# Kernel tuning notes

Measured on AMD Instinct MI355X. Metric: run time of the kernel, lower is better.

Reference implementation:

```python
import jax, jax.numpy as jnp
import numpy as np


def setup_inputs() -> dict:
    key = jax.random.key(0)
    k1, k2 = jax.random.split(key)
    x = jax.random.normal(k1, (16, 512, 64, 64), dtype=jnp.float32)
    gamma = jax.random.normal(k2, (1,), dtype=jnp.float32) * 0.05  # 'random_normal' init
    return {"x": x, "gamma": gamma}


def reference(x, gamma):
    # x: (B, C, H, W); code path is channels_last, C taken from x.shape[1]
    B, C, H, W = x.shape
    N = H * W
    # Reshape((-1, C)) is a flat row-major reshape -> (B, N, C)
    q = x.reshape(B, N, C)  # query == key == value (same tensor)
    # energy = matmul(query, key, transpose_a=True) -> (B, C, C)
    energy = jnp.einsum('bnc,bnd->bcd', q, q)
    # reduce_max(energy, axis=1, keepdims=True)[0]: max over axis 1 then take
    # FIRST BATCH element -> shape (1, C), broadcast against (B, C, C)
    mx = jnp.max(energy, axis=1, keepdims=True)[0]  # (1, C)
    energy_2 = mx - energy  # (B, C, C)
    # Keras Activation('softmax') -> softmax over last axis
    attention = jax.nn.softmax(energy_2, axis=-1)  # (B, C, C)
    # matmul(attention, value, transpose_b=True): (B,C,C) @ (B,C,N) -> (B,C,N)
    out = jnp.einsum('bcd,bnd->bcn', attention, q)
    # Reshape back to x.shape[1:] = (C, H, W) (flat reshape, N = H*W)
    out = out.reshape(B, C, H, W)
    return gamma * out + x
```

## Files before the change

kernel.cpp:

```cpp
#include <hip/hip_runtime.h>
#include <cstdint>

#define B_DIM 16
#define C_DIM 512
#define N_DIM 4096

typedef __bf16 bf16x8 __attribute__((ext_vector_type(8)));
typedef unsigned short u16x8 __attribute__((ext_vector_type(8)));
typedef unsigned short u16x4 __attribute__((ext_vector_type(4)));
typedef unsigned int u32x4 __attribute__((ext_vector_type(4)));
typedef unsigned int u32x2 __attribute__((ext_vector_type(2)));
typedef float f32x4 __attribute__((ext_vector_type(4)));

__device__ __forceinline__ bf16x8 as_bf(u16x8 v) { return __builtin_bit_cast(bf16x8, v); }

__device__ __forceinline__ unsigned pack_hi(unsigned ua, unsigned ub) {
    return __builtin_amdgcn_perm(ub, ua, 0x07060302u);
}
__device__ __forceinline__ unsigned rne_pack(float a, float b) {
    unsigned ua = __float_as_uint(a);
    ua += 0x7fffu + ((ua >> 16) & 1u);
    unsigned ub = __float_as_uint(b);
    ub += 0x7fffu + ((ub >> 16) & 1u);
    return pack_hi(ua, ub);
}

#define BT 128
#define BK 32
#define BKP 40

__global__ __launch_bounds__(256) void gram_kernel(const float* __restrict__ x,
                                                   float* __restrict__ part, int kshift) {
    const int nwg = 10 * gridDim.z;
    const int chunk = nwg >> 3;
    const int flat = blockIdx.x + 10 * blockIdx.z;
    const int swz = (flat & 7) * chunk + (flat >> 3);
    const int tile = swz % 10;
    const int z = swz / 10;
    const int s = z & ((1 << kshift) - 1);
    const int b = z >> kshift;
    static const int TI[10] = {0, 0, 0, 0, 1, 1, 1, 2, 2, 3};
    static const int TJ[10] = {0, 1, 2, 3, 1, 2, 3, 2, 3, 3};
    const int c0 = TI[tile] * BT;
    const int d0 = TJ[tile] * BT;
    const bool diag = (c0 == d0);

    const float* __restrict__ Q = x + (size_t)b * (N_DIM * C_DIM);
    float* __restrict__ E = part + ((size_t)s * B_DIM + b) * (C_DIM * C_DIM);

    __shared__ unsigned short lAh[BT][BKP];
    __shared__ unsigned short lAl[BT][BKP];
    __shared__ unsigned short lBh[BT][BKP];
    __shared__ unsigned short lBl[BT][BKP];

    const int tid = threadIdx.x;
    const int lane = tid & 63;
    const int w = tid >> 6;
    const int moff = (w & 1) * 64;
    const int noff = (w >> 1) * 64;
    const int frow = lane & 15;
    const int fk = (lane >> 4) * 8;

    f32x4 acc[4][4];
#pragma unroll
    for (int m = 0; m < 4; ++m)
#pragma unroll
        for (int n = 0; n < 4; ++n) acc[m][n] = (f32x4){0.f, 0.f, 0.f, 0.f};

    const int cc = tid & 127;
    const int kh = tid >> 7;

    const int klen = N_DIM >> kshift;
    const float* gA = Q + (size_t)(s * klen + kh * 16) * C_DIM + (c0 + cc);
    const float* gB = Q + (size_t)(s * klen + kh * 16) * C_DIM + (d0 + cc);

    const unsigned short(*pBh)[BKP] = diag ? lAh : lBh;
    const unsigned short(*pBl)[BKP] = diag ? lAl : lBl;

    float av[16], bv[16];
#pragma unroll
    for (int i = 0; i < 16; ++i) av[i] = gA[(size_t)i * C_DIM];
    if (!diag) {
#pragma unroll
        for (int i = 0; i < 16; ++i) bv[i] = gB[(size_t)i * C_DIM];
    }
    gA += (size_t)BK * C_DIM;
    gB += (size_t)BK * C_DIM;

    const int T = klen / BK;
    for (int t = 0; t < T; ++t) {
        u32x4 ah[2], al[2], bh[2], bl[2];
#pragma unroll
        for (int g = 0; g < 2; ++g)
#pragma unroll
            for (int p = 0; p < 4; ++p) {
                const int j = g * 8 + p * 2;
                unsigned u0 = __float_as_uint(av[j]), u1 = __float_as_uint(av[j + 1]);
                ah[g][p] = pack_hi(u0, u1);
                float r0 = av[j] - __uint_as_float(u0 & 0xffff0000u);
                float r1 = av[j + 1] - __uint_as_float(u1 & 0xffff0000u);
                al[g][p] = pack_hi(__float_as_uint(r0), __float_as_uint(r1));
            }
        if (!diag) {
#pragma unroll
            for (int g = 0; g < 2; ++g)
#pragma unroll
                for (int p = 0; p < 4; ++p) {
                    const int j = g * 8 + p * 2;
                    unsigned u0 = __float_as_uint(bv[j]), u1 = __float_as_uint(bv[j + 1]);
                    bh[g][p] = pack_hi(u0, u1);
                    float r0 = bv[j] - __uint_as_float(u0 & 0xffff0000u);
                    float r1 = bv[j + 1] - __uint_as_float(u1 & 0xffff0000u);
                    bl[g][p] = pack_hi(__float_as_uint(r0), __float_as_uint(r1));
                }
        }

        __syncthreads();
        *(u16x8*)&lAh[cc][kh * 16]     = __builtin_bit_cast(u16x8, ah[0]);
        *(u16x8*)&lAh[cc][kh * 16 + 8] = __builtin_bit_cast(u16x8, ah[1]);
        *(u16x8*)&lAl[cc][kh * 16]     = __builtin_bit_cast(u16x8, al[0]);
        *(u16x8*)&lAl[cc][kh * 16 + 8] = __builtin_bit_cast(u16x8, al[1]);
        if (!diag) {
            *(u16x8*)&lBh[cc][kh * 16]     = __builtin_bit_cast(u16x8, bh[0]);
            *(u16x8*)&lBh[cc][kh * 16 + 8] = __builtin_bit_cast(u16x8, bh[1]);
            *(u16x8*)&lBl[cc][kh * 16]     = __builtin_bit_cast(u16x8, bl[0]);
            *(u16x8*)&lBl[cc][kh * 16 + 8] = __builtin_bit_cast(u16x8, bl[1]);
        }
        __syncthreads();

        if (t + 1 < T) {
#pragma unroll
            for (int i = 0; i < 16; ++i) av[i] = gA[(size_t)i * C_DIM];
            if (!diag) {
#pragma unroll
                for (int i = 0; i < 16; ++i) bv[i] = gB[(size_t)i * C_DIM];
            }
            gA += (size_t)BK * C_DIM;
            gB += (size_t)BK * C_DIM;
        }

        bf16x8 fbh[4], fbl[4];
#pragma unroll
        for (int n = 0; n < 4; ++n) {
            fbh[n] = as_bf(*(const u16x8*)&pBh[noff + n * 16 + frow][fk]);
            fbl[n] = as_bf(*(const u16x8*)&pBl[noff + n * 16 + frow][fk]);
        }
#pragma unroll
        for (int m = 0; m < 4; ++m) {
            bf16x8 fah = as_bf(*(const u16x8*)&lAh[moff + m * 16 + frow][fk]);
            bf16x8 fal = as_bf(*(const u16x8*)&lAl[moff + m * 16 + frow][fk]);
#pragma unroll
            for (int n = 0; n < 4; ++n) {
                acc[m][n] = __builtin_amdgcn_mfma_f32_16x16x32_bf16(fah, fbh[n], acc[m][n], 0, 0, 0);
                acc[m][n] = __builtin_amdgcn_mfma_f32_16x16x32_bf16(fah, fbl[n], acc[m][n], 0, 0, 0);
                acc[m][n] = __builtin_amdgcn_mfma_f32_16x16x32_bf16(fal, fbh[n], acc[m][n], 0, 0, 0);
            }
        }
    }

#pragma unroll
    for (int m = 0; m < 4; ++m)
#pragma unroll
        for (int n = 0; n < 4; ++n) {
            const int r = c0 + moff + m * 16 + (lane >> 4) * 4;
            const int col = d0 + noff + n * 16 + frow;
#pragma unroll
            for (int i = 0; i < 4; ++i)
                E[(size_t)(r + i) * C_DIM + col] = acc[m][n][i];
        }
    if (!diag) {
#pragma unroll
        for (int m = 0; m < 4; ++m)
#pragma unroll
            for (int n = 0; n < 4; ++n) {
                const int r = c0 + moff + m * 16 + (lane >> 4) * 4;
                const int col = d0 + noff + n * 16 + frow;
#pragma unroll
                for (int i = 0; i < 4; ++i)
                    E[(size_t)col * C_DIM + (r + i)] = acc[m][n][i];
            }
    }
}

__global__ __launch_bounds__(256) void colmax1(const float* __restrict__ part,
                                               float* __restrict__ pmax, int sk) {
    const int d = blockIdx.x * 256 + threadIdx.x;
    const int cg = blockIdx.y;
    const size_t PS = (size_t)B_DIM * C_DIM * C_DIM;
    float m = -3.4e38f;
    for (int c = cg * 16; c < cg * 16 + 16; ++c) {
        float e = 0.f;
        for (int s = 0; s < sk; ++s) e += part[(size_t)s * PS + (size_t)c * C_DIM + d];
        m = fmaxf(m, e);
    }
    pmax[cg * C_DIM + d] = m;
}

__global__ __launch_bounds__(256) void colmax2(const float* __restrict__ pmax,
                                               float* __restrict__ mx) {
    const int d = blockIdx.x * 256 + threadIdx.x;
    float m = pmax[d];
#pragma unroll
    for (int g = 1; g < 32; ++g) m = fmaxf(m, pmax[g * C_DIM + d]);
    mx[d] = m;
}

__global__ __launch_bounds__(256) void softmax_kernel(float* __restrict__ part,
                                                      const float* __restrict__ mx, int sk) {
    const int wid = blockIdx.x * 4 + (threadIdx.x >> 6);
    const int lane = threadIdx.x & 63;
    const size_t PS = (size_t)B_DIM * C_DIM * C_DIM;

    f32x4 ea = (f32x4){0.f, 0.f, 0.f, 0.f}, eb = ea;
    for (int s = 0; s < sk; ++s) {
        const f32x4* row = (const f32x4*)(part + (size_t)s * PS + (size_t)wid * C_DIM + lane * 8);
        ea += row[0];
        eb += row[1];
    }
    f32x4 ma = *(const f32x4*)&mx[lane * 8];
    f32x4 mb = *(const f32x4*)&mx[lane * 8 + 4];

    float v[8];
#pragma unroll
    for (int j = 0; j < 4; ++j) v[j] = ma[j] - ea[j];
#pragma unroll
    for (int j = 0; j < 4; ++j) v[4 + j] = mb[j] - eb[j];

    float rm = v[0];
#pragma unroll
    for (int j = 1; j < 8; ++j) rm = fmaxf(rm, v[j]);
#pragma unroll
    for (int st = 1; st < 64; st <<= 1) rm = fmaxf(rm, __shfl_xor(rm, st));

    float p[8];
    float sum = 0.f;
#pragma unroll
    for (int j = 0; j < 8; ++j) {
        p[j] = expf(v[j] - rm);
        sum += p[j];
    }
#pragma unroll
    for (int st = 1; st < 64; st <<= 1) sum += __shfl_xor(sum, st);

    const float inv = 1.f / sum;
    u32x4 o;
#pragma unroll
    for (int q = 0; q < 4; ++q) o[q] = rne_pack(p[2 * q] * inv, p[2 * q + 1] * inv);
    unsigned short* arow = (unsigned short*)part + (size_t)wid * 1024 + 512;
    *(u16x8*)&arow[lane * 8] = __builtin_bit_cast(u16x8, o);
}

__global__ __launch_bounds__(256) void gemm2_kernel(const unsigned short* __restrict__ att16,
                                                    const float* __restrict__ x,
                                                    const float* __restrict__ gamma,
                                                    float* __restrict__ out) {
    const int flat = blockIdx.x;
    const int swz = (flat & 7) * 256 + (flat >> 3);
    const int c0 = (swz & 3) * BT;
    const int n0 = ((swz >> 2) & 31) * BT;
    const int b = swz >> 7;

    const float* __restrict__ Q = x + (size_t)b * (N_DIM * C_DIM);
    float* __restrict__ Ob = out + (size_t)b * (C_DIM * N_DIM);
    const unsigned short* __restrict__ Ab = att16 + (size_t)(b * C_DIM + c0) * 1024 + 512;

    __shared__ unsigned short lA[2][BT][BKP];
    __shared__ unsigned short lB[2][BT][BKP];

    const int tid = threadIdx.x;
    const int lane = tid & 63;
    const int w = tid >> 6;
    const int moff = (w & 1) * 64;
    const int noff = (w >> 1) * 64;
    const int frow = lane & 15;
    const int fq = lane >> 4;
    const int fk = fq * 8;

    f32x4 acc[4][4];
#pragma unroll
    for (int m = 0; m < 4; ++m)
#pragma unroll
        for (int n = 0; n < 4; ++n) acc[m][n] = (f32x4){0.f, 0.f, 0.f, 0.f};

    const int ar = tid >> 2;
    const int ak = (tid & 3) * 8;
    const int br = tid >> 3;
    const int bk = (tid & 7) * 4;

    u16x8 pa[2];
    float4 rb[4];
#pragma unroll
    for (int i = 0; i < 2; ++i)
        pa[i] = *(const u16x8*)&Ab[(size_t)(ar + 64 * i) * 1024 + ak];
#pragma unroll
    for (int i = 0; i < 4; ++i)
        rb[i] = *(const float4*)&Q[(size_t)(n0 + br + 32 * i) * C_DIM + bk];
#pragma unroll
    for (int i = 0; i < 2; ++i)
        *(u16x8*)&lA[0][ar + 64 * i][ak] = pa[i];
#pragma unroll
    for (int i = 0; i < 4; ++i) {
        u32x2 pk = {pack_hi(__float_as_uint(rb[i].x), __float_as_uint(rb[i].y)),
                    pack_hi(__float_as_uint(rb[i].z), __float_as_uint(rb[i].w))};
        *(u16x4*)&lB[0][br + 32 * i][bk] = __builtin_bit_cast(u16x4, pk);
    }

    int cur = 0;
    for (int t = 0; t < 16; ++t) {
        __syncthreads();
        if (t < 15) {
            const int k1 = (t + 1) * BK;
#pragma unroll
            for (int i = 0; i < 2; ++i)
                pa[i] = *(const u16x8*)&Ab[(size_t)(ar + 64 * i) * 1024 + k1 + ak];
#pragma unroll
            for (int i = 0; i < 4; ++i)
                rb[i] = *(const float4*)&Q[(size_t)(n0 + br + 32 * i) * C_DIM + k1 + bk];
        }

        bf16x8 fb[4];
#pragma unroll
        for (int n = 0; n < 4; ++n)
            fb[n] = as_bf(*(const u16x8*)&lB[cur][noff + n * 16 + frow][fk]);
#pragma unroll
        for (int m = 0; m < 4; ++m) {
            const bf16x8 fa = as_bf(*(const u16x8*)&lA[cur][moff + m * 16 + frow][fk]);
#pragma unroll
            for (int n = 0; n < 4; ++n)
                acc[m][n] = __builtin_amdgcn_mfma_f32_16x16x32_bf16(fa, fb[n], acc[m][n], 0, 0, 0);
        }

        if (t < 15) {
            const int nb = cur ^ 1;
#pragma unroll
            for (int i = 0; i < 2; ++i)
                *(u16x8*)&lA[nb][ar + 64 * i][ak] = pa[i];
#pragma unroll
            for (int i = 0; i < 4; ++i) {
                u32x2 pk = {pack_hi(__float_as_uint(rb[i].x), __float_as_uint(rb[i].y)),
                            pack_hi(__float_as_uint(rb[i].z), __float_as_uint(rb[i].w))};
                *(u16x4*)&lB[nb][br + 32 * i][bk] = __builtin_bit_cast(u16x4, pk);
            }
        }
        cur ^= 1;
    }

    const float g = gamma[0];
#pragma unroll
    for (int m = 0; m < 4; ++m)
#pragma unroll
        for (int n = 0; n < 4; ++n) {
            const int r = c0 + moff + m * 16 + fq * 4;
            const int col = n0 + noff + n * 16 + frow;
#pragma unroll
            for (int i = 0; i < 4; ++i) {
                const size_t idx = (size_t)(r + i) * N_DIM + col;
                Ob[idx] = g * acc[m][n][i] + Q[idx];
            }
        }
}

extern "C" void kernel_launch(void* const* d_in, const int* in_sizes, int n_in,
                              void* d_out, int out_size, void* d_ws, size_t ws_size,
                              hipStream_t stream) {
    const float* x = (const float*)d_in[0];
    const float* gamma = (const float*)d_in[1];
    float* out = (float*)d_out;

    const size_t HDR = 128 * 1024;
    const size_t PSZ = (size_t)B_DIM * C_DIM * C_DIM * sizeof(float);
    int kshift = 0;
    if (ws_size >= HDR + 8 * PSZ) kshift = 3;
    else if (ws_size >= HDR + 4 * PSZ) kshift = 2;
    else if (ws_size >= HDR + 2 * PSZ) kshift = 1;
    const int SK = 1 << kshift;

    float* mx = (float*)d_ws;
    float* pmax = mx + C_DIM;
    float* part = (float*)((char*)d_ws + HDR);

    dim3 g1(10, 1, B_DIM * SK);
    gram_kernel<<<g1, 256, 0, stream>>>(x, part, kshift);

    colmax1<<<dim3(2, 32), 256, 0, stream>>>(part, pmax, SK);
    colmax2<<<2, 256, 0, stream>>>(pmax, mx);

    softmax_kernel<<<(B_DIM * C_DIM) / 4, 256, 0, stream>>>(part, mx, SK);

    gemm2_kernel<<<2048, 256, 0, stream>>>((const unsigned short*)part, x, gamma, out);
}
```

Before: 246.7 us.

## Emit bf16 copy of x in gram kernel; feed gemm2 via direct global-to-LDS loads

The diagonal gram tiles now write a truncated bf16 copy of x to workspace as a side effect. gemm2 reads that half-size copy instead of reading fp32 x and converting it, and it loads both operands with global_load_lds straight into an XOR-swizzled, unpadded shared buffer. This halves gemm2's B-operand traffic and removes register staging and conversion work. The cost is extra global writes in the gram kernel and a larger workspace, which may lower the split-K factor. The bf16 copy also uses truncation rather than round-to-nearest.

New measurement: 344.3 us. 39.5% more time.

```diff
diff --git a/kernel.cpp b/kernel.cpp
--- a/kernel.cpp
+++ b/kernel.cpp
@@ -25,12 +25,19 @@
     return pack_hi(ua, ub);
 }
 
+__device__ __forceinline__ void gload_lds16(const void* g, void* l) {
+    __builtin_amdgcn_global_load_lds((const __attribute__((address_space(1))) void*)g,
+                                     (__attribute__((address_space(3))) void*)l, 16, 0, 0);
+}
+
 #define BT 128
 #define BK 32
 #define BKP 40
 
 __global__ __launch_bounds__(256) void gram_kernel(const float* __restrict__ x,
-                                                   float* __restrict__ part, int kshift) {
+                                                   float* __restrict__ part,
+                                                   unsigned short* __restrict__ xbf,
+                                                   int kshift) {
     const int nwg = 10 * gridDim.z;
     const int chunk = nwg >> 3;
     const int flat = blockIdx.x + 10 * blockIdx.z;
@@ -73,6 +80,8 @@
     const int klen = N_DIM >> kshift;
     const float* gA = Q + (size_t)(s * klen + kh * 16) * C_DIM + (c0 + cc);
     const float* gB = Q + (size_t)(s * klen + kh * 16) * C_DIM + (d0 + cc);
+    unsigned short* gW = xbf + (size_t)b * (N_DIM * C_DIM) +
+                         (size_t)(s * klen + kh * 16) * C_DIM + (c0 + cc);
 
     const unsigned short(*pBh)[BKP] = diag ? lAh : lBh;
     const unsigned short(*pBl)[BKP] = diag ? lAl : lBl;
@@ -113,6 +122,12 @@
                     float r1 = bv[j + 1] - __uint_as_float(u1 & 0xffff0000u);
                     bl[g][p] = pack_hi(__float_as_uint(r0), __float_as_uint(r1));
                 }
+        } else {
+#pragma unroll
+            for (int i = 0; i < 16; ++i)
+                gW[(size_t)i * C_DIM] =
+                    (unsigned short)(__float_as_uint(av[i]) >> 16);
+            gW += (size_t)BK * C_DIM;
         }
 
         __syncthreads();
@@ -251,6 +266,7 @@
 }
 
 __global__ __launch_bounds__(256) void gemm2_kernel(const unsigned short* __restrict__ att16,
+                                                    const unsigned short* __restrict__ xbf,
                                                     const float* __restrict__ x,
                                                     const float* __restrict__ gamma,
                                                     float* __restrict__ out) {
@@ -260,12 +276,13 @@
     const int n0 = ((swz >> 2) & 31) * BT;
     const int b = swz >> 7;
 
-    const float* __restrict__ Q = x + (size_t)b * (N_DIM * C_DIM);
+    const float* __restrict__ Xf = x + (size_t)b * (N_DIM * C_DIM);
     float* __restrict__ Ob = out + (size_t)b * (C_DIM * N_DIM);
     const unsigned short* __restrict__ Ab = att16 + (size_t)(b * C_DIM + c0) * 1024 + 512;
-
-    __shared__ unsigned short lA[2][BT][BKP];
-    __shared__ unsigned short lB[2][BT][BKP];
+    const unsigned short* __restrict__ Bb = xbf + ((size_t)b * N_DIM + n0) * C_DIM;
+
+    __shared__ unsigned short lA[2][BT][BK];
+    __shared__ unsigned short lB[2][BT][BK];
 
     const int tid = threadIdx.x;
     const int lane = tid & 63;
@@ -274,7 +291,10 @@
     const int noff = (w >> 1) * 64;
     const int frow = lane & 15;
     const int fq = lane >> 4;
-    const int fk = fq * 8;
+    const int sfr = (fq ^ (frow & 3)) * 8;
+
+    const int sr = tid >> 2;
+    const int sc = (((tid & 3) ^ ((tid >> 2) & 3)) << 3);
 
     f32x4 acc[4][4];
 #pragma unroll
@@ -282,66 +302,42 @@
 #pragma unroll
         for (int n = 0; n < 4; ++n) acc[m][n] = (f32x4){0.f, 0.f, 0.f, 0.f};
 
-    const int ar = tid >> 2;
-    const int ak = (tid & 3) * 8;
-    const int br = tid >> 3;
-    const int bk = (tid & 7) * 4;
-
-    u16x8 pa[2];
-    float4 rb[4];
-#pragma unroll
-    for (int i = 0; i < 2; ++i)
-        pa[i] = *(const u16x8*)&Ab[(size_t)(ar + 64 * i) * 1024 + ak];
-#pragma unroll
-    for (int i = 0; i < 4; ++i)
-        rb[i] = *(const float4*)&Q[(size_t)(n0 + br + 32 * i) * C_DIM + bk];
-#pragma unroll
-    for (int i = 0; i < 2; ++i)
-        *(u16x8*)&lA[0][ar + 64 * i][ak] = pa[i];
-#pragma unroll
-    for (int i = 0; i < 4; ++i) {
-        u32x2 pk = {pack_hi(__float_as_uint(rb[i].x), __float_as_uint(rb[i].y)),
-                    pack_hi(__float_as_uint(rb[i].z), __float_as_uint(rb[i].w))};
-        *(u16x4*)&lB[0][br + 32 * i][bk] = __builtin_bit_cast(u16x4, pk);
-    }
+#pragma unroll
+    for (int i = 0; i < 2; ++i) {
+        gload_lds16(&Ab[(size_t)(sr + 64 * i) * 1024 + sc],
+                    &lA[0][0][0] + (size_t)(tid + 256 * i) * 8);
+        gload_lds16(&Bb[(size_t)(sr + 64 * i) * C_DIM + sc],
+                    &lB[0][0][0] + (size_t)(tid + 256 * i) * 8);
+    }
+    __syncthreads();
 
     int cur = 0;
     for (int t = 0; t < 16; ++t) {
-        __syncthreads();
         if (t < 15) {
             const int k1 = (t + 1) * BK;
-#pragma unroll
-            for (int i = 0; i < 2; ++i)
-                pa[i] = *(const u16x8*)&Ab[(size_t)(ar + 64 * i) * 1024 + k1 + ak];
-#pragma unroll
-            for (int i = 0; i < 4; ++i)
-                rb[i] = *(const float4*)&Q[(size_t)(n0 + br + 32 * i) * C_DIM + k1 + bk];
+            const int nb = cur ^ 1;
+#pragma unroll
+            for (int i = 0; i < 2; ++i) {
+                gload_lds16(&Ab[(size_t)(sr + 64 * i) * 1024 + k1 + sc],
+                            &lA[nb][0][0] + (size_t)(tid + 256 * i) * 8);
+                gload_lds16(&Bb[(size_t)(sr + 64 * i) * C_DIM + k1 + sc],
+                            &lB[nb][0][0] + (size_t)(tid + 256 * i) * 8);
+            }
         }
 
         bf16x8 fb[4];
 #pragma unroll
         for (int n = 0; n < 4; ++n)
-            fb[n] = as_bf(*(const u16x8*)&lB[cur][noff + n * 16 + frow][fk]);
+            fb[n] = as_bf(*(const u16x8*)&lB[cur][noff + n * 16 + frow][sfr]);
 #pragma unroll
         for (int m = 0; m < 4; ++m) {
-            const bf16x8 fa = as_bf(*(const u16x8*)&lA[cur][moff + m * 16 + frow][fk]);
+            const bf16x8 fa = as_bf(*(const u16x8*)&lA[cur][moff + m * 16 + frow][sfr]);
 #pragma unroll
             for (int n = 0; n < 4; ++n)
                 acc[m][n] = __builtin_amdgcn_mfma_f32_16x16x32_bf16(fa, fb[n], acc[m][n], 0, 0, 0);
         }
 
-        if (t < 15) {
-            const int nb = cur ^ 1;
-#pragma unroll
-            for (int i = 0; i < 2; ++i)
-                *(u16x8*)&lA[nb][ar + 64 * i][ak] = pa[i];
-#pragma unroll
-            for (int i = 0; i < 4; ++i) {
-                u32x2 pk = {pack_hi(__float_as_uint(rb[i].x), __float_as_uint(rb[i].y)),
-                            pack_hi(__float_as_uint(rb[i].z), __float_as_uint(rb[i].w))};
-                *(u16x4*)&lB[nb][br + 32 * i][bk] = __builtin_bit_cast(u16x4, pk);
-            }
-        }
+        __syncthreads();
         cur ^= 1;
     }
 
@@ -355,7 +351,7 @@
 #pragma unroll
             for (int i = 0; i < 4; ++i) {
                 const size_t idx = (size_t)(r + i) * N_DIM + col;
-                Ob[idx] = g * acc[m][n][i] + Q[idx];
+                Ob[idx] = g * acc[m][n][i] + Xf[idx];
             }
         }
 }
@@ -368,24 +364,26 @@
     float* out = (float*)d_out;
 
     const size_t HDR = 128 * 1024;
+    const size_t XBF = (size_t)B_DIM * N_DIM * C_DIM * sizeof(unsigned short);
     const size_t PSZ = (size_t)B_DIM * C_DIM * C_DIM * sizeof(float);
     int kshift = 0;
-    if (ws_size >= HDR + 8 * PSZ) kshift = 3;
-    else if (ws_size >= HDR + 4 * PSZ) kshift = 2;
-    else if (ws_size >= HDR + 2 * PSZ) kshift = 1;
+    if (ws_size >= HDR + XBF + 8 * PSZ) kshift = 3;
+    else if (ws_size >= HDR + XBF + 4 * PSZ) kshift = 2;
+    else if (ws_size >= HDR + XBF + 2 * PSZ) kshift = 1;
     const int SK = 1 << kshift;
 
     float* mx = (float*)d_ws;
     float* pmax = mx + C_DIM;
-    float* part = (float*)((char*)d_ws + HDR);
+    unsigned short* xbf = (unsigned short*)((char*)d_ws + HDR);
+    float* part = (float*)((char*)d_ws + HDR + XBF);
 
     dim3 g1(10, 1, B_DIM * SK);
-    gram_kernel<<<g1, 256, 0, stream>>>(x, part, kshift);
+    gram_kernel<<<g1, 256, 0, stream>>>(x, part, xbf, kshift);
 
     colmax1<<<dim3(2, 32), 256, 0, stream>>>(part, pmax, SK);
     colmax2<<<2, 256, 0, stream>>>(pmax, mx);
 
     softmax_kernel<<<(B_DIM * C_DIM) / 4, 256, 0, stream>>>(part, mx, SK);
 
-    gemm2_kernel<<<2048, 256, 0, stream>>>((const unsigned short*)part, x, gamma, out);
-}
+    gemm2_kernel<<<2048, 256, 0, stream>>>((const unsigned short*)part, xbf, x, gamma, out);
+}
```
